# Optimization experiments

Hardware: AMD Instinct MI355X
Metric: run time of the kernel (lower is better)

The kernel has to match this reference:

```python
import jax, jax.numpy as jnp
import numpy as np

EPS = 0.5
MIN_PTS = 10


def setup_inputs() -> dict:
    key = jax.random.key(0)
    point_features = jax.random.normal(key, (4, 8192, 16), dtype=jnp.float32)
    return {"point_features": point_features}


def reference(point_features) -> jnp.ndarray:
    # torch.cdist(x, x): pairwise Euclidean distances, shape [B, N, N]
    x = point_features
    sq = jnp.sum(x * x, axis=-1)                      # [B, N]
    # squared distances via ||a||^2 + ||b||^2 - 2 a.b
    d2 = sq[:, :, None] + sq[:, None, :] - 2.0 * jnp.einsum('bnd,bmd->bnm', x, x)
    dist = jnp.sqrt(jnp.maximum(d2, 0.0))             # [B, N, N]
    # neighbors = 1 where dist < eps (includes self, dist==0)
    neighbor_count = jnp.sum(dist < EPS, axis=2)      # [B, N] int
    # final_clusters starts at 0; points with too few neighbors marked -1 (noise)
    final_clusters = jnp.where(neighbor_count < MIN_PTS, -1, 0).astype(jnp.int32)
    return final_clusters
```

## Files before the change

### kernel.cpp

```cpp
#include <hip/hip_runtime.h>


constexpr int Np = 8192;
constexpr int Bb = 4;
constexpr int MIN_PTS = 10;
constexpr int JS = 16;
constexpr int RF = 4;
constexpr int JW = Np / JS;
constexpr int NT = JW / 16;

typedef __bf16 bf16x8 __attribute__((ext_vector_type(8)));
typedef float  f32x4  __attribute__((ext_vector_type(4)));

__global__ __launch_bounds__(256)
void dbscan_prep(const float* __restrict__ x, __bf16* __restrict__ aug,
                 int* __restrict__ out) {
    const int p = blockIdx.x * 256 + threadIdx.x;
    const float4* src = (const float4*)(x + (size_t)p * 16);
    float4 v0 = src[0], v1 = src[1], v2 = src[2], v3 = src[3];
    float vv[16];
    vv[0]=v0.x; vv[1]=v0.y; vv[2]=v0.z; vv[3]=v0.w;
    vv[4]=v1.x; vv[5]=v1.y; vv[6]=v1.z; vv[7]=v1.w;
    vv[8]=v2.x; vv[9]=v2.y; vv[10]=v2.z; vv[11]=v2.w;
    vv[12]=v3.x; vv[13]=v3.y; vv[14]=v3.z; vv[15]=v3.w;
    float s = 0.f;
#pragma unroll
    for (int k = 0; k < 16; k++) s = fmaf(vv[k], vv[k], s);
    const float g = 0.5f * s - 0.125f;
    bf16x8 h0, h1, h2;
#pragma unroll
    for (int k = 0; k < 8; k++) { h0[k] = (__bf16)vv[k]; h1[k] = (__bf16)vv[k+8]; }
    h2[0] = (__bf16)1.0f; h2[1] = (__bf16)(-g);
#pragma unroll
    for (int k = 2; k < 8; k++) h2[k] = (__bf16)0.0f;
    bf16x8* dst = (bf16x8*)(aug + (size_t)p * 24);
    dst[0] = h0; dst[1] = h1; dst[2] = h2;
    out[p] = 0;
}

__global__ __launch_bounds__(256, 8)
void dbscan_count(const __bf16* __restrict__ aug, int* __restrict__ out) {
    const int W    = blockIdx.x * 4 + (threadIdx.x >> 6);
    const int lane = threadIdx.x & 63;
    const int m    = lane & 15;
    const int q    = lane >> 4;
    const int js   = W >> 9;
    const int chunk= W & 511;
    const int b    = chunk >> 7;
    const int ibase= (chunk & 127) * 64;
    const size_t pbase = (size_t)b * Np;

    bf16x8 af[RF];
#pragma unroll
    for (int f = 0; f < RF; f++) {
        const __bf16* ap = aug + (pbase + ibase + f*16 + m) * 24 + q * 8;
        bf16x8 a = *(const bf16x8*)ap;
        if (q == 2) { __bf16 t = a[0]; a[0] = a[1]; a[1] = t; }
        if (q == 3) {
#pragma unroll
            for (int k = 0; k < 8; k++) a[k] = (__bf16)0.0f;
        }
        af[f] = a;
    }

    const __bf16* bbase = aug + (pbase + (size_t)js * JW + m) * 24 + q * 8;
    const f32x4 zacc = {0.f, 0.f, 0.f, 0.f};
    int cnt[16];
#pragma unroll
    for (int i = 0; i < 16; i++) cnt[i] = 0;

    bf16x8 bc = *(const bf16x8*)bbase;
#pragma unroll 2
    for (int t = 0; t < NT; t++) {
        const int tn = (t + 1) & (NT - 1);
        bf16x8 bn = *(const bf16x8*)(bbase + (size_t)tn * 16 * 24);
#pragma unroll
        for (int f = 0; f < RF; f++) {
            f32x4 acc = __builtin_amdgcn_mfma_f32_16x16x32_bf16(af[f], bc, zacc, 0, 0, 0);
            cnt[f*4+0] += (acc[0] > 0.0f) ? 1 : 0;
            cnt[f*4+1] += (acc[1] > 0.0f) ? 1 : 0;
            cnt[f*4+2] += (acc[2] > 0.0f) ? 1 : 0;
            cnt[f*4+3] += (acc[3] > 0.0f) ? 1 : 0;
        }
        bc = bn;
    }

#pragma unroll
    for (int i = 0; i < 16; i++) {
        int v = cnt[i];
        v += __shfl_xor(v, 1);
        v += __shfl_xor(v, 2);
        v += __shfl_xor(v, 4);
        v += __shfl_xor(v, 8);
        cnt[i] = v;
    }
    if (m == 0) {
        int* ob = out + pbase + ibase;
#pragma unroll
        for (int f = 0; f < RF; f++)
#pragma unroll
            for (int r = 0; r < 4; r++)
                atomicAdd(&ob[f*16 + q*4 + r], cnt[f*4+r]);
    }
}

__global__ __launch_bounds__(256)
void dbscan_classify(int* __restrict__ out) {
    const int p = blockIdx.x * 256 + threadIdx.x;
    out[p] = (out[p] < MIN_PTS) ? -1 : 0;
}

extern "C" void kernel_launch(void* const* d_in, const int* in_sizes, int n_in,
                              void* d_out, int out_size, void* d_ws, size_t ws_size,
                              hipStream_t stream) {
    const float* x = (const float*)d_in[0];
    int* out = (int*)d_out;
    __bf16* aug = (__bf16*)d_ws;

    dbscan_prep<<<dim3(Bb * Np / 256), dim3(256), 0, stream>>>(x, aug, out);
    dbscan_count<<<dim3(Bb * (Np / 64) * JS / 4), dim3(256), 0, stream>>>(aug, out);
    dbscan_classify<<<dim3(Bb * Np / 256), dim3(256), 0, stream>>>(out);
}
```

Measured before the change: 82.95 us.

## Stage shared column tile in LDS and share it across four row waves

The count kernel now assigns one block to a 256-row by 512-column tile. The block cooperatively loads the column points into LDS, laid out so each 16-point group is contiguous per k-chunk, and all four waves read their B fragments from LDS instead of each wave fetching them from global memory. This cuts redundant global/L2 traffic for the B operand. The cost is a barrier, 24KB of LDS per block, and a lower occupancy hint (6 instead of 8).

```diff
diff --git a/kernel.cpp b/kernel.cpp
--- a/kernel.cpp
+++ b/kernel.cpp
@@ -5,8 +5,9 @@
 constexpr int Bb = 4;
 constexpr int MIN_PTS = 10;
 constexpr int JS = 16;
+constexpr int JW = Np / JS;
+constexpr int ICH = 256;
 constexpr int RF = 4;
-constexpr int JW = Np / JS;
 constexpr int NT = JW / 16;
 
 typedef __bf16 bf16x8 __attribute__((ext_vector_type(8)));
@@ -38,22 +39,38 @@
     out[p] = 0;
 }
 
-__global__ __launch_bounds__(256, 8)
+__global__ __launch_bounds__(256, 6)
 void dbscan_count(const __bf16* __restrict__ aug, int* __restrict__ out) {
-    const int W    = blockIdx.x * 4 + (threadIdx.x >> 6);
     const int lane = threadIdx.x & 63;
+    const int w    = threadIdx.x >> 6;
     const int m    = lane & 15;
     const int q    = lane >> 4;
-    const int js   = W >> 9;
-    const int chunk= W & 511;
-    const int b    = chunk >> 7;
-    const int ibase= (chunk & 127) * 64;
+    const int blk  = blockIdx.x;
+    const int b    = blk >> 9;
+    const int ic   = (blk >> 4) & 31;
+    const int js   = blk & 15;
     const size_t pbase = (size_t)b * Np;
+    const int ibase = ic * ICH;
+    const int jbase = js * JW;
+
+    __shared__ __bf16 ldsB[NT * 48 * 8];
+
+    {
+        const __bf16* src = aug + (pbase + jbase) * 24;
+#pragma unroll
+        for (int it = 0; it < 6; it++) {
+            const int c = threadIdx.x + it * 256;
+            const int p = c / 3;
+            const int r = c - p * 3;
+            bf16x8 v = *(const bf16x8*)(src + (size_t)c * 8);
+            *(bf16x8*)(ldsB + (((p >> 4) * 48) + r * 16 + (p & 15)) * 8) = v;
+        }
+    }
 
     bf16x8 af[RF];
 #pragma unroll
     for (int f = 0; f < RF; f++) {
-        const __bf16* ap = aug + (pbase + ibase + f*16 + m) * 24 + q * 8;
+        const __bf16* ap = aug + (pbase + ibase + w * 64 + f * 16 + m) * 24 + q * 8;
         bf16x8 a = *(const bf16x8*)ap;
         if (q == 2) { __bf16 t = a[0]; a[0] = a[1]; a[1] = t; }
         if (q == 3) {
@@ -63,17 +80,20 @@
         af[f] = a;
     }
 
-    const __bf16* bbase = aug + (pbase + (size_t)js * JW + m) * 24 + q * 8;
+    __syncthreads();
+
+    const __bf16* bptr = ldsB + (q < 3 ? (q * 16 + m) * 8 : 0);
+
     const f32x4 zacc = {0.f, 0.f, 0.f, 0.f};
     int cnt[16];
 #pragma unroll
     for (int i = 0; i < 16; i++) cnt[i] = 0;
 
-    bf16x8 bc = *(const bf16x8*)bbase;
+    bf16x8 bc = *(const bf16x8*)bptr;
 #pragma unroll 2
     for (int t = 0; t < NT; t++) {
         const int tn = (t + 1) & (NT - 1);
-        bf16x8 bn = *(const bf16x8*)(bbase + (size_t)tn * 16 * 24);
+        bf16x8 bn = *(const bf16x8*)(bptr + tn * 48 * 8);
 #pragma unroll
         for (int f = 0; f < RF; f++) {
             f32x4 acc = __builtin_amdgcn_mfma_f32_16x16x32_bf16(af[f], bc, zacc, 0, 0, 0);
@@ -95,7 +115,7 @@
         cnt[i] = v;
     }
     if (m == 0) {
-        int* ob = out + pbase + ibase;
+        int* ob = out + pbase + ibase + w * 64;
 #pragma unroll
         for (int f = 0; f < RF; f++)
 #pragma unroll
@@ -118,6 +138,6 @@
     __bf16* aug = (__bf16*)d_ws;
 
     dbscan_prep<<<dim3(Bb * Np / 256), dim3(256), 0, stream>>>(x, aug, out);
-    dbscan_count<<<dim3(Bb * (Np / 64) * JS / 4), dim3(256), 0, stream>>>(aug, out);
+    dbscan_count<<<dim3(Bb * 32 * JS), dim3(256), 0, stream>>>(aug, out);
     dbscan_classify<<<dim3(Bb * Np / 256), dim3(256), 0, stream>>>(out);
 }
```

Result: faster. 80.74 us (-2.7%).
